# Kernel optimization log

Hardware: AMD Instinct MI355X
Metric: run time of the kernel (lower is better)

## Reference

```python
import jax, jax.numpy as jnp
import numpy as np

N_NODES = 100000
IN_F = 32
OUT_F = 32
EDGE_F = 16
N_EDGES = 400000
BN_EPS = 1e-5
LEAKY_SLOPE = 0.01


def setup_inputs() -> dict:
    key = jax.random.key(0)
    ks = jax.random.split(key, 8)
    node_feature = jax.random.normal(ks[0], (N_NODES, IN_F), dtype=jnp.float32)
    edge_feature = jax.random.normal(ks[1], (N_EDGES, EDGE_F), dtype=jnp.float32)
    nn_w = jax.random.normal(ks[2], (EDGE_F, IN_F * OUT_F), dtype=jnp.float32) * (1.0 / np.sqrt(EDGE_F))
    nn_b = jax.random.normal(ks[3], (IN_F * OUT_F,), dtype=jnp.float32) * 0.01
    root = jax.random.normal(ks[4], (IN_F, OUT_F), dtype=jnp.float32) * (1.0 / np.sqrt(IN_F))
    bias = jax.random.normal(ks[5], (OUT_F,), dtype=jnp.float32) * 0.01
    gamma = jnp.ones((OUT_F,), dtype=jnp.float32)
    beta = jnp.zeros((OUT_F,), dtype=jnp.float32)
    edge_index = jax.random.randint(ks[6], (2, N_EDGES), 0, N_NODES, dtype=jnp.int64)
    return {
        "node_feature": node_feature,
        "edge_feature": edge_feature,
        "nn_w": nn_w,
        "nn_b": nn_b,
        "root": root,
        "bias": bias,
        "gamma": gamma,
        "beta": beta,
        "edge_index": edge_index,
    }


def reference(node_feature, edge_feature, nn_w, nn_b, root, bias, gamma, beta, edge_index):
    src, dst = edge_index[0], edge_index[1]  # messages flow src -> dst (PyG source_to_target)
    # Edge MLP: per-edge weight matrix [E, IN_F, OUT_F]
    edge_w = (edge_feature @ nn_w + nn_b).reshape(-1, IN_F, OUT_F)
    # Gather source node features and apply per-edge matmul: [E, OUT_F]
    msg = jnp.einsum("ei,eio->eo", node_feature[src], edge_w)
    # Scatter-add aggregation at target nodes
    agg = jax.ops.segment_sum(msg, dst, num_segments=node_feature.shape[0])
    # Root transform + bias (NNConv root_weight=True, bias=True)
    h = agg + node_feature @ root + bias
    # BatchNorm1d (training mode: batch statistics over nodes, biased variance)
    mean = jnp.mean(h, axis=0)
    var = jnp.var(h, axis=0)
    h = (h - mean) * jax.lax.rsqrt(var + BN_EPS) * gamma + beta
    # LeakyReLU (default negative_slope = 0.01)
    return jnp.where(h >= 0, h, LEAKY_SLOPE * h)
```

## Files before the change

### kernel.cpp

```cpp
#include <hip/hip_runtime.h>

#define IN_F 32
#define OUT_F 32
#define EDGE_F 16
#define BN_EPS 1e-5f
#define SLOPE 0.01f

typedef _Float16 half_t;
typedef __attribute__((ext_vector_type(4))) _Float16 h4;

__global__ __launch_bounds__(256) void gemm_y_kernel(
    const float* __restrict__ x, const float* __restrict__ W,
    const float* __restrict__ b, const float* __restrict__ root,
    const float* __restrict__ bias, half_t* __restrict__ Y,
    float* __restrict__ out, int N) {
  __shared__ float xl[32][33];
  __shared__ float Wl[4 * 32 * 32];

  bool last = (blockIdx.y == 4);
  int f0 = blockIdx.y * 4;
  int n0 = blockIdx.x * 32;
  int tid = threadIdx.x;

  {
    int r = tid >> 3, p = tid & 7;
    int n = n0 + r;
    float4 v = make_float4(0.f, 0.f, 0.f, 0.f);
    if (n < N) v = *(const float4*)(x + (size_t)n * IN_F + p * 4);
    xl[r][p * 4 + 0] = v.x; xl[r][p * 4 + 1] = v.y;
    xl[r][p * 4 + 2] = v.z; xl[r][p * 4 + 3] = v.w;
  }
  {
    float4* Wl4 = (float4*)Wl;
#pragma unroll
    for (int k = 0; k < 4; ++k) {
      int idx = k * 256 + tid;
      int fi = idx >> 8;
      int rest = idx & 255;
      float4 v = make_float4(0.f, 0.f, 0.f, 0.f);
      if (!last)          v = *(const float4*)(W + (size_t)(f0 + fi) * 1024 + rest * 4);
      else if (fi == 0)   v = *(const float4*)(b + rest * 4);
      else if (fi == 1)   v = *(const float4*)(root + rest * 4);
      Wl4[idx] = v;
    }
  }
  __syncthreads();

  int nl = tid >> 3, oq = tid & 7;
  int n = n0 + nl;
  const float4* Wl4 = (const float4*)Wl;
  int nfi = last ? 2 : 4;
  for (int fi = 0; fi < nfi; ++fi) {
    float4 acc = make_float4(0.f, 0.f, 0.f, 0.f);
#pragma unroll
    for (int i = 0; i < IN_F; ++i) {
      float xi = xl[nl][i];
      float4 w = Wl4[(fi * 32 + i) * 8 + oq];
      acc.x = fmaf(xi, w.x, acc.x);
      acc.y = fmaf(xi, w.y, acc.y);
      acc.z = fmaf(xi, w.z, acc.z);
      acc.w = fmaf(xi, w.w, acc.w);
    }
    if (n < N) {
      if (!last || fi == 0) {
        h4 hv;
        hv[0] = (half_t)acc.x; hv[1] = (half_t)acc.y;
        hv[2] = (half_t)acc.z; hv[3] = (half_t)acc.w;
        *(h4*)(Y + (size_t)n * 544 + (f0 + fi) * 32 + oq * 4) = hv;
      } else {
        float4 bv = *(const float4*)(bias + oq * 4);
        acc.x += bv.x; acc.y += bv.y; acc.z += bv.z; acc.w += bv.w;
        *(float4*)(out + (size_t)n * OUT_F + oq * 4) = acc;
      }
    }
  }
}

__global__ __launch_bounds__(256) void edge_light_kernel(
    const half_t* __restrict__ Y, const float* __restrict__ ef,
    const int* __restrict__ ei, float* __restrict__ agg, int E) {
  __shared__ float efl[32][17];
  __shared__ float msg[32][33];
  __shared__ int dstl[32];

  int e0 = blockIdx.x * 32;
  int t = threadIdx.x;
  int el = t >> 3, oq = t & 7;
  int e = e0 + el;
  bool ev = (e < E);

  if (t < 128) {
    int ee = e0 + (t >> 2);
    int q = t & 3;
    float4 v = make_float4(0.f, 0.f, 0.f, 0.f);
    if (ee < E) v = *(const float4*)(ef + (size_t)ee * EDGE_F + q * 4);
    efl[t >> 2][q * 4 + 0] = v.x; efl[t >> 2][q * 4 + 1] = v.y;
    efl[t >> 2][q * 4 + 2] = v.z; efl[t >> 2][q * 4 + 3] = v.w;
  }
  if (t < 32) {
    int ee = e0 + t;
    dstl[t] = (ee < E) ? ei[E + ee] : -1;
  }
  int s = ev ? ei[e] : 0;
  __syncthreads();

  const half_t* yrow = Y + (size_t)s * 544 + oq * 4;
  float acc[4];
  {
    h4 v = *(const h4*)(yrow + 16 * 32);
#pragma unroll
    for (int j = 0; j < 4; ++j) acc[j] = (float)v[j];
  }
#pragma unroll
  for (int f = 0; f < EDGE_F; ++f) {
    float m = efl[el][f];
    h4 v = *(const h4*)(yrow + f * 32);
#pragma unroll
    for (int j = 0; j < 4; ++j) acc[j] = fmaf(m, (float)v[j], acc[j]);
  }
#pragma unroll
  for (int j = 0; j < 4; ++j) msg[el][oq * 4 + j] = acc[j];
  __syncthreads();

  int d = dstl[el];
  if (d >= 0) {
    float* dp = agg + (size_t)d * OUT_F;
#pragma unroll
    for (int j = 0; j < 4; ++j)
      atomicAdd(dp + j * 8 + oq, msg[el][j * 8 + oq]);
  }
}

__global__ __launch_bounds__(256) void node_root_kernel(
    const float* __restrict__ x, const float* __restrict__ root,
    const float* __restrict__ bias, float* __restrict__ agg, int N) {
  __shared__ float rl[IN_F * OUT_F];
  __shared__ float bl[OUT_F];
  for (int t = threadIdx.x; t < IN_F * OUT_F; t += blockDim.x) rl[t] = root[t];
  if (threadIdx.x < OUT_F) bl[threadIdx.x] = bias[threadIdx.x];
  __syncthreads();
  int n = blockIdx.x * blockDim.x + threadIdx.x;
  bool valid = (n < N);
  int nu = valid ? n : 0;
  float xr[IN_F];
  const float4* xp = (const float4*)(x + (size_t)nu * IN_F);
#pragma unroll
  for (int q = 0; q < IN_F / 4; ++q) {
    float4 v = xp[q];
    xr[q * 4 + 0] = v.x; xr[q * 4 + 1] = v.y; xr[q * 4 + 2] = v.z; xr[q * 4 + 3] = v.w;
  }
  float acc[OUT_F];
#pragma unroll
  for (int o = 0; o < OUT_F; ++o) acc[o] = bl[o];
#pragma unroll
  for (int i = 0; i < IN_F; ++i) {
    float xi = xr[i];
#pragma unroll
    for (int o = 0; o < OUT_F; ++o) acc[o] = fmaf(xi, rl[i * OUT_F + o], acc[o]);
  }
  if (valid) {
    float4* op = (float4*)(agg + (size_t)n * OUT_F);
#pragma unroll
    for (int q = 0; q < OUT_F / 4; ++q)
      op[q] = make_float4(acc[q * 4 + 0], acc[q * 4 + 1], acc[q * 4 + 2], acc[q * 4 + 3]);
  }
}

__global__ __launch_bounds__(256) void edge_kernel(
    const float* __restrict__ x, const float* __restrict__ ef,
    const float* __restrict__ W, const float* __restrict__ b,
    const int* __restrict__ ei, float* __restrict__ agg, int E) {
  __shared__ float Wl[EDGE_F * IN_F * OUT_F];
  int e = blockIdx.x * blockDim.x + threadIdx.x;
  bool valid = (e < E);
  int eu = valid ? e : 0;
  int s = ei[eu];
  int d = ei[E + eu];
  float efr[EDGE_F];
  {
    const float4* ep = (const float4*)(ef + (size_t)eu * EDGE_F);
#pragma unroll
    for (int q = 0; q < EDGE_F / 4; ++q) {
      float4 v = ep[q];
      efr[q * 4 + 0] = v.x; efr[q * 4 + 1] = v.y;
      efr[q * 4 + 2] = v.z; efr[q * 4 + 3] = v.w;
    }
  }
  const float* xrow = x + (size_t)s * IN_F;
  float acc[OUT_F];
#pragma unroll
  for (int o = 0; o < OUT_F; ++o) acc[o] = 0.f;
  for (int t = threadIdx.x; t < IN_F * OUT_F; t += 256) Wl[t] = b[t];
  __syncthreads();
  for (int i = 0; i < IN_F; ++i) {
    float xi = xrow[i];
    const float* br = &Wl[i * OUT_F];
#pragma unroll
    for (int o = 0; o < OUT_F; ++o) acc[o] = fmaf(xi, br[o], acc[o]);
  }
  __syncthreads();
  for (int t = threadIdx.x; t < EDGE_F * IN_F * OUT_F / 4; t += 256)
    ((float4*)Wl)[t] = ((const float4*)W)[t];
  __syncthreads();
  for (int i = 0; i < IN_F; ++i) {
    float xi = xrow[i];
#pragma unroll
    for (int f = 0; f < EDGE_F; ++f) {
      float m = efr[f] * xi;
      const float* wr = &Wl[(f * IN_F + i) * OUT_F];
#pragma unroll
      for (int o = 0; o < OUT_F; ++o) acc[o] = fmaf(m, wr[o], acc[o]);
    }
  }
  if (valid) {
    float* dp = agg + (size_t)d * OUT_F;
#pragma unroll
    for (int o = 0; o < OUT_F; ++o) atomicAdd(dp + o, acc[o]);
  }
}

__global__ __launch_bounds__(256) void bn_stats_kernel(
    const float* __restrict__ h, float* __restrict__ stats, int total) {
  int t = blockIdx.x * blockDim.x + threadIdx.x;
  int stride = gridDim.x * blockDim.x;
  float s = 0.f, s2 = 0.f;
  for (int idx = t; idx < total; idx += stride) {
    float v = h[idx];
    s += v;
    s2 = fmaf(v, v, s2);
  }
  __shared__ float ls[256], ls2[256];
  ls[threadIdx.x] = s;
  ls2[threadIdx.x] = s2;
  __syncthreads();
  if (threadIdx.x < 32) {
    float a = ls[threadIdx.x], a2 = ls2[threadIdx.x];
    for (int j = 32 + threadIdx.x; j < 256; j += 32) { a += ls[j]; a2 += ls2[j]; }
    atomicAdd(&stats[threadIdx.x], a);
    atomicAdd(&stats[32 + threadIdx.x], a2);
  }
}

__global__ __launch_bounds__(256) void bn_apply_kernel(
    float* __restrict__ h, const float* __restrict__ stats,
    const float* __restrict__ gamma, const float* __restrict__ beta,
    int total, float invN) {
  int t = blockIdx.x * blockDim.x + threadIdx.x;
  int i4 = t * 4;
  if (i4 >= total) return;
  float4 v = *(const float4*)(h + i4);
  float r[4] = {v.x, v.y, v.z, v.w};
  int o0 = i4 & 31;
#pragma unroll
  for (int j = 0; j < 4; ++j) {
    int o = o0 + j;
    float m = stats[o] * invN;
    float var = fmaf(-m, m, stats[32 + o] * invN);
    float sc = rsqrtf(var + BN_EPS) * gamma[o];
    float val = (r[j] - m) * sc + beta[o];
    r[j] = val >= 0.f ? val : SLOPE * val;
  }
  *(float4*)(h + i4) = make_float4(r[0], r[1], r[2], r[3]);
}

extern "C" void kernel_launch(void* const* d_in, const int* in_sizes, int n_in,
                              void* d_out, int out_size, void* d_ws, size_t ws_size,
                              hipStream_t stream) {
  const float* x     = (const float*)d_in[0];
  const float* ef    = (const float*)d_in[1];
  const float* W     = (const float*)d_in[2];
  const float* b     = (const float*)d_in[3];
  const float* root  = (const float*)d_in[4];
  const float* bias  = (const float*)d_in[5];
  const float* gamma = (const float*)d_in[6];
  const float* beta  = (const float*)d_in[7];
  const int*   ei    = (const int*)d_in[8];

  float* out = (float*)d_out;
  float* stats = (float*)d_ws;
  half_t* Y = (half_t*)((char*)d_ws + 1024);

  int N = in_sizes[0] / IN_F;
  int E = in_sizes[1] / EDGE_F;
  int total = N * OUT_F;
  size_t need = 1024 + (size_t)N * 544 * sizeof(half_t);

  hipMemsetAsync(stats, 0, 64 * sizeof(float), stream);

  if (ws_size >= need) {
    gemm_y_kernel<<<dim3((N + 31) / 32, 5), 256, 0, stream>>>(x, W, b, root, bias, Y, out, N);
    edge_light_kernel<<<(E + 31) / 32, 256, 0, stream>>>(Y, ef, ei, out, E);
  } else {
    node_root_kernel<<<(N + 255) / 256, 256, 0, stream>>>(x, root, bias, out, N);
    edge_kernel<<<(E + 255) / 256, 256, 0, stream>>>(x, ef, W, b, ei, out, E);
  }
  bn_stats_kernel<<<1024, 256, 0, stream>>>(out, stats, total);
  bn_apply_kernel<<<(total / 4 + 255) / 256, 256, 0, stream>>>(out, stats, gamma, beta, total, 1.0f / (float)N);
}
```

Before: 215.4 us.

## Compute node-weight GEMM with MFMA f16 and prefetch Y rows before barrier

```diff
diff --git a/kernel.cpp b/kernel.cpp
--- a/kernel.cpp
+++ b/kernel.cpp
@@ -8,69 +8,77 @@
 
 typedef _Float16 half_t;
 typedef __attribute__((ext_vector_type(4))) _Float16 h4;
-
-__global__ __launch_bounds__(256) void gemm_y_kernel(
-    const float* __restrict__ x, const float* __restrict__ W,
-    const float* __restrict__ b, const float* __restrict__ root,
+typedef __attribute__((ext_vector_type(8))) _Float16 f16x8;
+typedef __attribute__((ext_vector_type(4))) float f32x4;
+
+#define BCOLS 576
+#define BSTRIDE_B 80
+
+__global__ __launch_bounds__(256) void prep_bt_kernel(
+    const float* __restrict__ W, const float* __restrict__ b,
+    const float* __restrict__ root, half_t* __restrict__ BtG) {
+  for (int idx = threadIdx.x; idx < BCOLS * 32; idx += 256) {
+    int col = idx >> 5, k = idx & 31;
+    float v;
+    if (col < 512) {
+      int f = col >> 5, o = col & 31;
+      v = W[(size_t)f * 1024 + k * 32 + o];
+    } else if (col < 544) {
+      v = b[k * 32 + (col - 512)];
+    } else {
+      v = root[k * 32 + (col - 544)];
+    }
+    BtG[(size_t)col * 32 + k] = (half_t)v;
+  }
+}
+
+__global__ __launch_bounds__(256) void gemm_y_mfma_kernel(
+    const float* __restrict__ x, const half_t* __restrict__ BtG,
     const float* __restrict__ bias, half_t* __restrict__ Y,
     float* __restrict__ out, int N) {
-  __shared__ float xl[32][33];
-  __shared__ float Wl[4 * 32 * 32];
-
-  bool last = (blockIdx.y == 4);
-  int f0 = blockIdx.y * 4;
-  int n0 = blockIdx.x * 32;
+  __shared__ char BtL[BCOLS * BSTRIDE_B];
+
   int tid = threadIdx.x;
-
-  {
-    int r = tid >> 3, p = tid & 7;
-    int n = n0 + r;
-    float4 v = make_float4(0.f, 0.f, 0.f, 0.f);
-    if (n < N) v = *(const float4*)(x + (size_t)n * IN_F + p * 4);
-    xl[r][p * 4 + 0] = v.x; xl[r][p * 4 + 1] = v.y;
-    xl[r][p * 4 + 2] = v.z; xl[r][p * 4 + 3] = v.w;
-  }
-  {
-    float4* Wl4 = (float4*)Wl;
-#pragma unroll
-    for (int k = 0; k < 4; ++k) {
-      int idx = k * 256 + tid;
-      int fi = idx >> 8;
-      int rest = idx & 255;
-      float4 v = make_float4(0.f, 0.f, 0.f, 0.f);
-      if (!last)          v = *(const float4*)(W + (size_t)(f0 + fi) * 1024 + rest * 4);
-      else if (fi == 0)   v = *(const float4*)(b + rest * 4);
-      else if (fi == 1)   v = *(const float4*)(root + rest * 4);
-      Wl4[idx] = v;
-    }
-  }
-  __syncthreads();
-
-  int nl = tid >> 3, oq = tid & 7;
-  int n = n0 + nl;
-  const float4* Wl4 = (const float4*)Wl;
-  int nfi = last ? 2 : 4;
-  for (int fi = 0; fi < nfi; ++fi) {
-    float4 acc = make_float4(0.f, 0.f, 0.f, 0.f);
-#pragma unroll
-    for (int i = 0; i < IN_F; ++i) {
-      float xi = xl[nl][i];
-      float4 w = Wl4[(fi * 32 + i) * 8 + oq];
-      acc.x = fmaf(xi, w.x, acc.x);
-      acc.y = fmaf(xi, w.y, acc.y);
-      acc.z = fmaf(xi, w.z, acc.z);
-      acc.w = fmaf(xi, w.w, acc.w);
-    }
-    if (n < N) {
-      if (!last || fi == 0) {
-        h4 hv;
-        hv[0] = (half_t)acc.x; hv[1] = (half_t)acc.y;
-        hv[2] = (half_t)acc.z; hv[3] = (half_t)acc.w;
-        *(h4*)(Y + (size_t)n * 544 + (f0 + fi) * 32 + oq * 4) = hv;
-      } else {
-        float4 bv = *(const float4*)(bias + oq * 4);
-        acc.x += bv.x; acc.y += bv.y; acc.z += bv.z; acc.w += bv.w;
-        *(float4*)(out + (size_t)n * OUT_F + oq * 4) = acc;
+  for (int t = tid; t < BCOLS * 4; t += 256) {
+    int col = t >> 2, part = t & 3;
+    *(float4*)(BtL + col * BSTRIDE_B + part * 16) =
+        *(const float4*)((const char*)BtG + col * 64 + part * 16);
+  }
+  __syncthreads();
+
+  int wv = tid >> 6, lane = tid & 63;
+  int lr = lane & 15, kg = lane >> 4;
+  int n0 = blockIdx.x * 64 + wv * 16;
+  int row = n0 + lr;
+
+  f16x8 a;
+  if (row < N) {
+    float4 u0 = *(const float4*)(x + (size_t)row * 32 + kg * 8);
+    float4 u1 = *(const float4*)(x + (size_t)row * 32 + kg * 8 + 4);
+    a[0] = (half_t)u0.x; a[1] = (half_t)u0.y; a[2] = (half_t)u0.z; a[3] = (half_t)u0.w;
+    a[4] = (half_t)u1.x; a[5] = (half_t)u1.y; a[6] = (half_t)u1.z; a[7] = (half_t)u1.w;
+  } else {
+    a = (f16x8)(half_t)0.f;
+  }
+
+  for (int ct = 0; ct < 36; ++ct) {
+    int col = ct * 16 + lr;
+    f16x8 bf = *(const f16x8*)(BtL + col * BSTRIDE_B + kg * 16);
+    f32x4 c = {0.f, 0.f, 0.f, 0.f};
+    c = __builtin_amdgcn_mfma_f32_16x16x32_f16(a, bf, c, 0, 0, 0);
+    if (col < 544) {
+#pragma unroll
+      for (int j = 0; j < 4; ++j) {
+        int n = n0 + kg * 4 + j;
+        if (n < N) Y[(size_t)n * 544 + col] = (half_t)c[j];
+      }
+    } else {
+      int o = col - 544;
+      float bv = bias[o];
+#pragma unroll
+      for (int j = 0; j < 4; ++j) {
+        int n = n0 + kg * 4 + j;
+        if (n < N) out[(size_t)n * OUT_F + o] = c[j] + bv;
       }
     }
   }
@@ -88,6 +96,7 @@
   int el = t >> 3, oq = t & 7;
   int e = e0 + el;
   bool ev = (e < E);
+  int s = ev ? ei[e] : 0;
 
   if (t < 128) {
     int ee = e0 + (t >> 2);
@@ -101,22 +110,22 @@
     int ee = e0 + t;
     dstl[t] = (ee < E) ? ei[E + ee] : -1;
   }
-  int s = ev ? ei[e] : 0;
-  __syncthreads();
 
   const half_t* yrow = Y + (size_t)s * 544 + oq * 4;
+  h4 yv[17];
+#pragma unroll
+  for (int f = 0; f < 17; ++f) yv[f] = *(const h4*)(yrow + f * 32);
+
+  __syncthreads();
+
   float acc[4];
-  {
-    h4 v = *(const h4*)(yrow + 16 * 32);
-#pragma unroll
-    for (int j = 0; j < 4; ++j) acc[j] = (float)v[j];
-  }
+#pragma unroll
+  for (int j = 0; j < 4; ++j) acc[j] = (float)yv[16][j];
 #pragma unroll
   for (int f = 0; f < EDGE_F; ++f) {
     float m = efl[el][f];
-    h4 v = *(const h4*)(yrow + f * 32);
-#pragma unroll
-    for (int j = 0; j < 4; ++j) acc[j] = fmaf(m, (float)v[j], acc[j]);
+#pragma unroll
+    for (int j = 0; j < 4; ++j) acc[j] = fmaf(m, (float)yv[f][j], acc[j]);
   }
 #pragma unroll
   for (int j = 0; j < 4; ++j) msg[el][oq * 4 + j] = acc[j];
@@ -278,17 +287,19 @@
 
   float* out = (float*)d_out;
   float* stats = (float*)d_ws;
-  half_t* Y = (half_t*)((char*)d_ws + 1024);
+  half_t* BtG = (half_t*)((char*)d_ws + 1024);
+  half_t* Y = (half_t*)((char*)d_ws + 1024 + 36864);
 
   int N = in_sizes[0] / IN_F;
   int E = in_sizes[1] / EDGE_F;
   int total = N * OUT_F;
-  size_t need = 1024 + (size_t)N * 544 * sizeof(half_t);
+  size_t need = 1024 + 36864 + (size_t)N * 544 * sizeof(half_t);
 
   hipMemsetAsync(stats, 0, 64 * sizeof(float), stream);
 
   if (ws_size >= need) {
-    gemm_y_kernel<<<dim3((N + 31) / 32, 5), 256, 0, stream>>>(x, W, b, root, bias, Y, out, N);
+    prep_bt_kernel<<<1, 256, 0, stream>>>(W, b, root, BtG);
+    gemm_y_mfma_kernel<<<(N + 63) / 64, 256, 0, stream>>>(x, BtG, bias, Y, out, N);
     edge_light_kernel<<<(E + 31) / 32, 256, 0, stream>>>(Y, ef, ei, out, E);
   } else {
     node_root_kernel<<<(N + 255) / 256, 256, 0, stream>>>(x, root, bias, out, N);
```

After: 190.2 us. 11.7% less time.
